# Optimization experiments

Measured on AMD Instinct MI355X. Metric: run time of the kernel, lower is better.

The kernel has to match this reference:

```python
import jax, jax.numpy as jnp
import numpy as np

# ---- problem constants (mirror AdjustInstanceArea __init__ args) ----
NUM_NODES = 2_000_000
NUM_MOVABLE = 1_500_000
NUM_FILLER = 400_000
NUM_NETS = 1_500_000
PINS_PER_NET = 4                       # uniform netpin_start = arange(0, P+1, 4)
NUM_PINS = NUM_NETS * PINS_PER_NET
XL, XH, YL, YH = 0.0, 1000.0, 0.0, 1000.0
NBX = NBY = 512
BIN_W = (XH - XL) / NBX
BIN_H = (YH - YL) / NBY
UNIT_H_CAP = 1.5                       # unit horizontal routing capacity
UNIT_V_CAP = 1.5                       # unit vertical routing capacity
MAX_RATE = 2.0                         # max_route_opt_adjust_rate
MIN_RATE = 1.0 / MAX_RATE
EPS = 1e-6


def setup_inputs() -> dict:
    key = jax.random.key(0)
    k = jax.random.split(key, 4)
    x = jax.random.uniform(k[0], (NUM_NODES,), jnp.float32, XL, XH - 4.0)
    y = jax.random.uniform(k[1], (NUM_NODES,), jnp.float32, YL, YH - 4.0)
    pos = jnp.concatenate([x, y])                      # [2*num_nodes], x then y

    # pins clustered around net centers (realistic small net bboxes)
    rng = np.random.default_rng(0)
    centers = rng.uniform(0.0, 1000.0, size=(NUM_NETS, 1, 2)).astype(np.float32)
    jit = rng.uniform(-20.0, 20.0, size=(NUM_NETS, PINS_PER_NET, 2)).astype(np.float32)
    ppos = np.clip(centers + jit, 0.0, 1000.0)         # [nets, pins_per_net, 2], in net order

    # flat_netpin: pin ids grouped by net; pin_pos indexed by pin id
    flat_netpin = rng.permutation(NUM_PINS).astype(np.int32)
    px = np.empty(NUM_PINS, np.float32); py = np.empty(NUM_PINS, np.float32)
    px[flat_netpin] = ppos[..., 0].reshape(-1)
    py[flat_netpin] = ppos[..., 1].reshape(-1)
    pin_pos = jnp.concatenate([jnp.asarray(px), jnp.asarray(py)])  # [2*num_pins]

    pin2net = jnp.asarray(np.repeat(np.arange(NUM_NETS, dtype=np.int32), PINS_PER_NET))

    node_size_x = jax.random.uniform(k[2], (NUM_NODES,), jnp.float32, 1.0, 4.0)
    node_size_y = jax.random.uniform(k[3], (NUM_NODES,), jnp.float32, 1.0, 4.0)
    return {"pos": pos, "pin_pos": pin_pos,
            "node_size_x": node_size_x, "node_size_y": node_size_y,
            "flat_netpin": jnp.asarray(flat_netpin), "pin2net": pin2net}


def _rect_accum(vals, blx, bly, bhx, bhy):
    """Accumulate vals over inclusive bin rectangles via difference map + 2D cumsum."""
    D = jnp.zeros((NBX + 1, NBY + 1), vals.dtype)
    D = D.at[blx, bly].add(vals)
    D = D.at[bhx + 1, bly].add(-vals)
    D = D.at[blx, bhy + 1].add(-vals)
    D = D.at[bhx + 1, bhy + 1].add(vals)
    return jnp.cumsum(jnp.cumsum(D, axis=0), axis=1)[:NBX, :NBY]


def reference(pos, pin_pos, node_size_x, node_size_y, flat_netpin, pin2net):
    # ---- InstanceRouteOptimizationArea: RUDY routing demand per bin ----
    px = pin_pos[:NUM_PINS][flat_netpin].reshape(NUM_NETS, PINS_PER_NET)
    py = pin_pos[NUM_PINS:][flat_netpin].reshape(NUM_NETS, PINS_PER_NET)
    net_xl = jnp.min(px, axis=1); net_xh = jnp.max(px, axis=1)
    net_yl = jnp.min(py, axis=1); net_yh = jnp.max(py, axis=1)
    bw = net_xh - net_xl
    bh = net_yh - net_yl
    barea = jnp.maximum(bw * bh, EPS)
    dens_h = bw / barea                                # horizontal wire density
    dens_v = bh / barea                                # vertical wire density

    blx = jnp.clip(jnp.floor((net_xl - XL) / BIN_W), 0, NBX - 1).astype(jnp.int32)
    bhx = jnp.clip(jnp.floor((net_xh - XL) / BIN_W), 0, NBX - 1).astype(jnp.int32)
    bly = jnp.clip(jnp.floor((net_yl - YL) / BIN_H), 0, NBY - 1).astype(jnp.int32)
    bhy = jnp.clip(jnp.floor((net_yh - YL) / BIN_H), 0, NBY - 1).astype(jnp.int32)

    util_h = _rect_accum(dens_h, blx, bly, bhx, bhy) / UNIT_H_CAP
    util_v = _rect_accum(dens_v, blx, bly, bhx, bhy) / UNIT_V_CAP

    # per-movable-node utilization (gather at node center bin)
    x = pos[:NUM_NODES]; y = pos[NUM_NODES:]
    nsx_m = node_size_x[:NUM_MOVABLE]; nsy_m = node_size_y[:NUM_MOVABLE]
    cx = x[:NUM_MOVABLE] + 0.5 * nsx_m
    cy = y[:NUM_MOVABLE] + 0.5 * nsy_m
    bix = jnp.clip(jnp.floor((cx - XL) / BIN_W), 0, NBX - 1).astype(jnp.int32)
    biy = jnp.clip(jnp.floor((cy - YL) / BIN_H), 0, NBY - 1).astype(jnp.int32)
    util = jnp.maximum(util_h[bix, biy], util_v[bix, biy])
    ratio = jnp.clip(util, MIN_RATE, MAX_RATE)

    area_old = nsx_m * nsy_m
    instance_route_area = area_old * ratio

    # ---- AdjustInstanceArea: rescale under max_total_area budget ----
    filler_area_old = jnp.sum(node_size_x[NUM_NODES - NUM_FILLER:] *
                              node_size_y[NUM_NODES - NUM_FILLER:])
    max_total_area = jnp.sum(area_old) + filler_area_old
    scale = jnp.minimum(1.0, max_total_area / jnp.maximum(jnp.sum(instance_route_area), EPS))
    new_area = instance_route_area * scale
    sr = jnp.sqrt(new_area / jnp.maximum(area_old, EPS))
    nsx_new = nsx_m * sr
    nsy_new = nsy_m * sr

    # keep cell centers fixed while resizing
    x_out = x.at[:NUM_MOVABLE].add(0.5 * (nsx_m - nsx_new))
    y_out = y.at[:NUM_MOVABLE].add(0.5 * (nsy_m - nsy_new))

    # fillers absorb leftover area budget
    fscale = jnp.sqrt(jnp.maximum(max_total_area - jnp.sum(new_area), 0.0) /
                      jnp.maximum(filler_area_old, EPS))
    nsx_out = node_size_x.at[:NUM_MOVABLE].set(nsx_new)
    nsx_out = nsx_out.at[NUM_NODES - NUM_FILLER:].multiply(fscale)
    nsy_out = node_size_y.at[:NUM_MOVABLE].set(nsy_new)
    nsy_out = nsy_out.at[NUM_NODES - NUM_FILLER:].multiply(fscale)

    return jnp.concatenate([x_out, y_out, nsx_out, nsy_out])  # [4*num_nodes]
```

## Files before the change

kernel.cpp:

```cpp
#include <hip/hip_runtime.h>
#include <hip/hip_fp16.h>
#include <math.h>

#define N_NODES   2000000
#define N_MOVABLE 1500000
#define N_FILLER  400000
#define N_NETS    1500000
#define N_PINS    (N_NETS * 4)
#define NB        512
#define NT        16
#define TILE      32
#define NBUCKET   (NT * NT)
#define CAP       10240
#define NSLICE    4
#define NMAPS     NSLICE
#define NPB       4096
#define RED_BLOCKS 1024

__device__ __forceinline__ int bin_idx(float v) {
    float b = floorf(v / 1.953125f);
    b = fminf(fmaxf(b, 0.0f), 511.0f);
    return (int)b;
}

__global__ void pack_kernel(const float* __restrict__ pin_pos,
                            float2* __restrict__ pp,
                            unsigned* __restrict__ g_ptr) {
    if (blockIdx.x == 0 && threadIdx.x < NBUCKET) g_ptr[threadIdx.x] = 0u;
    int i = blockIdx.x * blockDim.x + threadIdx.x;
    if (i >= N_PINS / 4) return;
    float4 a = reinterpret_cast<const float4*>(pin_pos)[i];
    float4 b = reinterpret_cast<const float4*>(pin_pos + N_PINS)[i];
    float4* o = reinterpret_cast<float4*>(pp + 4 * (size_t)i);
    o[0] = make_float4(a.x, b.x, a.y, b.y);
    o[1] = make_float4(a.z, b.z, a.w, b.w);
}

template <bool PACKED>
__device__ __forceinline__ uint2 make_rec(const float* __restrict__ pin_pos,
                                          const float2* __restrict__ pp,
                                          int4 fp, int* bucket) {
    float2 p0, p1, p2, p3;
    if (PACKED) {
        p0 = pp[fp.x]; p1 = pp[fp.y]; p2 = pp[fp.z]; p3 = pp[fp.w];
    } else {
        p0 = make_float2(pin_pos[fp.x], pin_pos[N_PINS + fp.x]);
        p1 = make_float2(pin_pos[fp.y], pin_pos[N_PINS + fp.y]);
        p2 = make_float2(pin_pos[fp.z], pin_pos[N_PINS + fp.z]);
        p3 = make_float2(pin_pos[fp.w], pin_pos[N_PINS + fp.w]);
    }
    float xl = fminf(fminf(p0.x, p1.x), fminf(p2.x, p3.x));
    float xh = fmaxf(fmaxf(p0.x, p1.x), fmaxf(p2.x, p3.x));
    float yl = fminf(fminf(p0.y, p1.y), fminf(p2.y, p3.y));
    float yh = fmaxf(fmaxf(p0.y, p1.y), fmaxf(p2.y, p3.y));
    float bw = xh - xl, bh = yh - yl;
    float barea = fmaxf(bw * bh, 1e-6f);
    float vh = fminf((bw / barea) * (1.0f / 1.5f), 60000.0f);
    float vv = fminf((bh / barea) * (1.0f / 1.5f), 60000.0f);
    unsigned blx = bin_idx(xl), bhx = bin_idx(xh);
    unsigned bly = bin_idx(yl), bhy = bin_idx(yh);
    *bucket = (int)((bly >> 5) * NT + (blx >> 5));
    __half2 h = __float22half2_rn(make_float2(vh, vv));
    uint2 r;
    r.x = *reinterpret_cast<unsigned*>(&h);
    r.y = blx | (bly << 9) | ((bhx + 1 - blx) << 18) | ((bhy + 1 - bly) << 23);
    return r;
}

template <bool PACKED>
__global__ __launch_bounds__(1024)
void gather_bin_kernel(const float* __restrict__ pin_pos,
                       const float2* __restrict__ pp,
                       const int*  __restrict__ fnp,
                       uint2* __restrict__ slab,
                       unsigned* __restrict__ g_ptr) {
    __shared__ unsigned hist[NBUCKET];
    __shared__ unsigned base[NBUCKET];
    int t = threadIdx.x;
    if (t < NBUCKET) hist[t] = 0;
    __syncthreads();

    int n0 = blockIdx.x * NPB + t;
    bool v[4]; int4 fp[4]; uint2 r[4]; int b[4]; unsigned rk[4];
    #pragma unroll
    for (int k = 0; k < 4; ++k) {
        int n = n0 + k * 1024;
        v[k] = (n < N_NETS);
        fp[k] = v[k] ? *reinterpret_cast<const int4*>(fnp + 4 * (size_t)n)
                     : make_int4(0, 0, 0, 0);
    }
    #pragma unroll
    for (int k = 0; k < 4; ++k) {
        b[k] = 0;
        if (v[k]) r[k] = make_rec<PACKED>(pin_pos, pp, fp[k], &b[k]);
    }
    #pragma unroll
    for (int k = 0; k < 4; ++k) {
        rk[k] = v[k] ? atomicAdd(&hist[b[k]], 1u) : 0u;
    }
    __syncthreads();
    if (t < NBUCKET) {
        unsigned c = hist[t];
        base[t] = c ? atomicAdd(&g_ptr[t], c) : 0u;
    }
    __syncthreads();
    #pragma unroll
    for (int k = 0; k < 4; ++k) {
        if (v[k]) {
            unsigned s = base[b[k]] + rk[k];
            if (s < CAP) slab[(size_t)b[k] * CAP + s] = r[k];
        }
    }
}

__device__ __forceinline__ void rec_process(uint2 r, int x0, int y0,
                                            float2* acc) {
    float2 v = __half22float2(*reinterpret_cast<const __half2*>(&r.x));
    unsigned g = r.y;
    int ax0 = (int)(g & 511u);
    int ay0 = (int)((g >> 9) & 511u);
    int ax1 = ax0 + (int)((g >> 18) & 31u);
    int ay1 = ay0 + (int)((g >> 23) & 31u);
    int X0 = ax0 - x0, Y0 = ay0 - y0;
    int X1 = ax1 - x0, Y1 = ay1 - y0;
    bool iX0 = (unsigned)X0 < TILE, iX1 = (unsigned)X1 < TILE;
    bool iY0 = (unsigned)Y0 < TILE, iY1 = (unsigned)Y1 < TILE;
    if (iX0 && iY0) { atomicAdd(&acc[X0 * TILE + Y0].x,  v.x); atomicAdd(&acc[X0 * TILE + Y0].y,  v.y); }
    if (iX1 && iY0) { atomicAdd(&acc[X1 * TILE + Y0].x, -v.x); atomicAdd(&acc[X1 * TILE + Y0].y, -v.y); }
    if (iX0 && iY1) { atomicAdd(&acc[X0 * TILE + Y1].x, -v.x); atomicAdd(&acc[X0 * TILE + Y1].y, -v.y); }
    if (iX1 && iY1) { atomicAdd(&acc[X1 * TILE + Y1].x,  v.x); atomicAdd(&acc[X1 * TILE + Y1].y,  v.y); }
}

__global__ __launch_bounds__(256)
void accum_kernel(const uint2* __restrict__ slab,
                  const unsigned* __restrict__ g_cnt,
                  float2* __restrict__ Dp) {
    __shared__ float2 acc[TILE * TILE];
    int wg = blockIdx.x;
    int sl = wg & (NSLICE - 1), tile = wg >> 2;
    int tx = tile & (NT - 1), ty = tile >> 4;
    int tid = threadIdx.x;

    for (int i = tid; i < TILE * TILE; i += 256) acc[i] = make_float2(0.f, 0.f);
    __syncthreads();

    int x0 = tx * TILE, y0 = ty * TILE;
    #pragma unroll
    for (int dy = -1; dy <= 0; ++dy) {
        int sy = ty + dy; if (sy < 0) continue;
        #pragma unroll
        for (int dx = -1; dx <= 0; ++dx) {
            int sx = tx + dx; if (sx < 0) continue;
            int sb = sy * NT + sx;
            unsigned cnt = min(g_cnt[sb], (unsigned)CAP);
            unsigned lo = (cnt * (unsigned)sl) >> 2;
            unsigned hi = (cnt * (unsigned)(sl + 1)) >> 2;
            const uint2* recs = slab + (size_t)sb * CAP;
            unsigned i = lo + tid;
            for (; i + 768 < hi; i += 1024) {
                uint2 r0 = recs[i];
                uint2 r1 = recs[i + 256];
                uint2 r2 = recs[i + 512];
                uint2 r3 = recs[i + 768];
                rec_process(r0, x0, y0, acc);
                rec_process(r1, x0, y0, acc);
                rec_process(r2, x0, y0, acc);
                rec_process(r3, x0, y0, acc);
            }
            for (; i < hi; i += 256) rec_process(recs[i], x0, y0, acc);
        }
    }
    __syncthreads();

    float2* D = Dp + (size_t)sl * NB * NB;
    for (int i = tid; i < TILE * TILE; i += 256) {
        int X = i >> 5, Y = i & 31;
        D[(size_t)(x0 + X) * NB + (y0 + Y)] = acc[i];
    }
}

__global__ __launch_bounds__(512)
void scanA_kernel(const float2* __restrict__ Dp, float2* __restrict__ S) {
    __shared__ float2 s[NB];
    int x = blockIdx.x, t = threadIdx.x;
    float2 a = make_float2(0.f, 0.f);
    #pragma unroll
    for (int m = 0; m < NMAPS; ++m) {
        float2 v = Dp[(size_t)m * NB * NB + (size_t)x * NB + t];
        a.x += v.x; a.y += v.y;
    }
    s[t] = a;
    __syncthreads();
    for (int off = 1; off < NB; off <<= 1) {
        float2 u = s[t];
        if (t >= off) { float2 w = s[t - off]; u.x += w.x; u.y += w.y; }
        __syncthreads();
        s[t] = u;
        __syncthreads();
    }
    S[(size_t)x * NB + t] = s[t];
}

__global__ __launch_bounds__(512)
void scanB_kernel(float2* __restrict__ S) {
    __shared__ float2 s[NB];
    int y = blockIdx.x, t = threadIdx.x;
    s[t] = S[(size_t)t * NB + y];
    __syncthreads();
    for (int off = 1; off < NB; off <<= 1) {
        float2 u = s[t];
        if (t >= off) { float2 w = s[t - off]; u.x += w.x; u.y += w.y; }
        __syncthreads();
        s[t] = u;
        __syncthreads();
    }
    S[(size_t)t * NB + y] = s[t];
}

__global__ __launch_bounds__(256)
void reduce_kernel(const float* __restrict__ pos,
                   const float* __restrict__ nsx,
                   const float* __restrict__ nsy,
                   const float2* __restrict__ S,
                   double* __restrict__ partials) {
    const int MQ = N_MOVABLE / 4;
    const int TQ = MQ + N_FILLER / 4;
    double a_old = 0.0, a_route = 0.0, a_fill = 0.0;
    int stride = gridDim.x * blockDim.x;
    for (int q = blockIdx.x * blockDim.x + threadIdx.x; q < TQ; q += stride) {
        if (q < MQ) {
            int i = 4 * q;
            float4 x4  = *reinterpret_cast<const float4*>(pos + i);
            float4 y4  = *reinterpret_cast<const float4*>(pos + N_NODES + i);
            float4 sx4 = *reinterpret_cast<const float4*>(nsx + i);
            float4 sy4 = *reinterpret_cast<const float4*>(nsy + i);
            float xs[4] = {x4.x, x4.y, x4.z, x4.w};
            float ys[4] = {y4.x, y4.y, y4.z, y4.w};
            float sxs[4] = {sx4.x, sx4.y, sx4.z, sx4.w};
            float sys[4] = {sy4.x, sy4.y, sy4.z, sy4.w};
            #pragma unroll
            for (int k = 0; k < 4; ++k) {
                int bx = bin_idx(xs[k] + 0.5f * sxs[k]);
                int by = bin_idx(ys[k] + 0.5f * sys[k]);
                float2 u2 = S[(size_t)bx * NB + by];
                float ratio = fminf(fmaxf(fmaxf(u2.x, u2.y), 0.5f), 2.0f);
                float area = sxs[k] * sys[k];
                a_old += (double)area;
                a_route += (double)(area * ratio);
            }
        } else {
            int j = (N_NODES - N_FILLER) + 4 * (q - MQ);
            float4 sx4 = *reinterpret_cast<const float4*>(nsx + j);
            float4 sy4 = *reinterpret_cast<const float4*>(nsy + j);
            a_fill += (double)(sx4.x * sy4.x + sx4.y * sy4.y +
                               sx4.z * sy4.z + sx4.w * sy4.w);
        }
    }
    for (int off = 32; off > 0; off >>= 1) {
        a_old   += __shfl_down(a_old, off);
        a_route += __shfl_down(a_route, off);
        a_fill  += __shfl_down(a_fill, off);
    }
    __shared__ double sd[4][3];
    int wid = threadIdx.x >> 6, lane = threadIdx.x & 63;
    if (lane == 0) { sd[wid][0] = a_old; sd[wid][1] = a_route; sd[wid][2] = a_fill; }
    __syncthreads();
    if (threadIdx.x == 0) {
        double s0 = 0, s1 = 0, s2 = 0;
        for (int w = 0; w < 4; ++w) { s0 += sd[w][0]; s1 += sd[w][1]; s2 += sd[w][2]; }
        partials[blockIdx.x * 3 + 0] = s0;
        partials[blockIdx.x * 3 + 1] = s1;
        partials[blockIdx.x * 3 + 2] = s2;
    }
}

__global__ __launch_bounds__(256)
void finish_kernel(const double* __restrict__ partials,
                   double* __restrict__ sums) {
    int t = threadIdx.x;
    double s0 = 0, s1 = 0, s2 = 0;
    for (int r = t; r < RED_BLOCKS; r += 256) {
        s0 += partials[r * 3 + 0];
        s1 += partials[r * 3 + 1];
        s2 += partials[r * 3 + 2];
    }
    for (int off = 32; off > 0; off >>= 1) {
        s0 += __shfl_down(s0, off);
        s1 += __shfl_down(s1, off);
        s2 += __shfl_down(s2, off);
    }
    __shared__ double sd[4][3];
    int wid = t >> 6, lane = t & 63;
    if (lane == 0) { sd[wid][0] = s0; sd[wid][1] = s1; sd[wid][2] = s2; }
    __syncthreads();
    if (t == 0) {
        double a = 0, b = 0, c = 0;
        for (int w = 0; w < 4; ++w) { a += sd[w][0]; b += sd[w][1]; c += sd[w][2]; }
        sums[0] = a; sums[1] = b; sums[2] = c;
    }
}

__global__ __launch_bounds__(256)
void final_kernel(const float* __restrict__ pos,
                  const float* __restrict__ nsx,
                  const float* __restrict__ nsy,
                  const float2* __restrict__ S,
                  const double* __restrict__ sums,
                  float* __restrict__ out) {
    double sum_area  = sums[0];
    double sum_route = sums[1];
    double fill_old  = sums[2];
    double max_total = sum_area + fill_old;

    float scale = fminf(1.0f, (float)(max_total / fmax(sum_route, 1e-6)));
    float sum_new = (float)(scale * (float)sum_route);
    float fscale = sqrtf(fmaxf((float)max_total - sum_new, 0.0f) /
                         fmaxf((float)fill_old, 1e-6f));

    int q = blockIdx.x * blockDim.x + threadIdx.x;
    if (q >= N_NODES / 4) return;
    int i = 4 * q;

    float4 x4  = *reinterpret_cast<const float4*>(pos + i);
    float4 y4  = *reinterpret_cast<const float4*>(pos + N_NODES + i);
    float4 sx4 = *reinterpret_cast<const float4*>(nsx + i);
    float4 sy4 = *reinterpret_cast<const float4*>(nsy + i);

    float xs[4] = {x4.x, x4.y, x4.z, x4.w};
    float ys[4] = {y4.x, y4.y, y4.z, y4.w};
    float sxs[4] = {sx4.x, sx4.y, sx4.z, sx4.w};
    float sys[4] = {sy4.x, sy4.y, sy4.z, sy4.w};

    if (i < N_MOVABLE) {
        #pragma unroll
        for (int k = 0; k < 4; ++k) {
            int bx = bin_idx(xs[k] + 0.5f * sxs[k]);
            int by = bin_idx(ys[k] + 0.5f * sys[k]);
            float2 u2 = S[(size_t)bx * NB + by];
            float ratio = fminf(fmaxf(fmaxf(u2.x, u2.y), 0.5f), 2.0f);
            float area = sxs[k] * sys[k];
            float new_area = area * ratio * scale;
            float sr = sqrtf(new_area / fmaxf(area, 1e-6f));
            float sx_new = sxs[k] * sr, sy_new = sys[k] * sr;
            xs[k] = xs[k] + 0.5f * (sxs[k] - sx_new);
            ys[k] = ys[k] + 0.5f * (sys[k] - sy_new);
            sxs[k] = sx_new; sys[k] = sy_new;
        }
    } else if (i >= N_NODES - N_FILLER) {
        #pragma unroll
        for (int k = 0; k < 4; ++k) { sxs[k] *= fscale; sys[k] *= fscale; }
    }

    *reinterpret_cast<float4*>(out + i)               = make_float4(xs[0], xs[1], xs[2], xs[3]);
    *reinterpret_cast<float4*>(out + N_NODES + i)     = make_float4(ys[0], ys[1], ys[2], ys[3]);
    *reinterpret_cast<float4*>(out + 2 * N_NODES + i) = make_float4(sxs[0], sxs[1], sxs[2], sxs[3]);
    *reinterpret_cast<float4*>(out + 3 * N_NODES + i) = make_float4(sys[0], sys[1], sys[2], sys[3]);
}

extern "C" void kernel_launch(void* const* d_in, const int* in_sizes, int n_in,
                              void* d_out, int out_size, void* d_ws, size_t ws_size,
                              hipStream_t stream) {
    const float* pos         = (const float*)d_in[0];
    const float* pin_pos     = (const float*)d_in[1];
    const float* nsx         = (const float*)d_in[2];
    const float* nsy         = (const float*)d_in[3];
    const int*   flat_netpin = (const int*)d_in[4];
    float* out = (float*)d_out;

    const size_t pp_b   = (size_t)N_PINS * sizeof(float2);
    const size_t slab_b = (size_t)NBUCKET * CAP * sizeof(uint2);
    const size_t dp_b   = (size_t)NMAPS * NB * NB * sizeof(float2);
    const size_t s_b    = (size_t)NB * NB * sizeof(float2);
    const size_t part_b = (size_t)RED_BLOCKS * 3 * sizeof(double);
    const size_t gp_b   = 4096;

    const size_t need_primary = pp_b + slab_b + gp_b + 256;

    char* base = (char*)d_ws;
    bool packed = (ws_size >= need_primary);

    float2* pp; uint2* slab; float2* Dp; float2* S;
    double* partials; double* sums; unsigned* g_ptr;
    if (packed) {
        pp       = (float2*)base;
        Dp       = (float2*)base;
        S        = (float2*)(base + dp_b);
        partials = (double*)(base + dp_b + s_b);
        sums     = (double*)(base + dp_b + s_b + part_b);
        slab     = (uint2*)(base + pp_b);
        g_ptr    = (unsigned*)(base + pp_b + slab_b);
    } else {
        pp       = nullptr;
        slab     = (uint2*)base;
        Dp       = (float2*)(base + slab_b);
        S        = (float2*)(base + slab_b + dp_b);
        partials = (double*)(base + slab_b + dp_b + s_b);
        sums     = (double*)(base + slab_b + dp_b + s_b + part_b);
        g_ptr    = (unsigned*)(base + slab_b + dp_b + s_b + part_b + 64);
    }

    const int GB_BLOCKS = (N_NETS + NPB - 1) / NPB;
    if (packed) {
        pack_kernel<<<(N_PINS / 4 + 255) / 256, 256, 0, stream>>>(pin_pos, pp, g_ptr);
        gather_bin_kernel<true><<<GB_BLOCKS, 1024, 0, stream>>>(pin_pos, pp, flat_netpin, slab, g_ptr);
    } else {
        hipMemsetAsync(g_ptr, 0, NBUCKET * sizeof(unsigned), stream);
        gather_bin_kernel<false><<<GB_BLOCKS, 1024, 0, stream>>>(pin_pos, nullptr, flat_netpin, slab, g_ptr);
    }

    accum_kernel <<<NBUCKET * NSLICE, 256, 0, stream>>>(slab, g_ptr, Dp);
    scanA_kernel <<<NB, 512, 0, stream>>>(Dp, S);
    scanB_kernel <<<NB, 512, 0, stream>>>(S);
    reduce_kernel<<<RED_BLOCKS, 256, 0, stream>>>(pos, nsx, nsy, S, partials);
    finish_kernel<<<1, 256, 0, stream>>>(partials, sums);
    final_kernel <<<(N_NODES / 4 + 255) / 256, 256, 0, stream>>>(pos, nsx, nsy, S, sums, out);
}
```

Measured before the change: 239.0 us.

## Replace random pin gather with three-pass bucketed pin gather and net reduction

```diff
diff --git a/kernel.cpp b/kernel.cpp
--- a/kernel.cpp
+++ b/kernel.cpp
@@ -14,8 +14,19 @@
 #define CAP       10240
 #define NSLICE    4
 #define NMAPS     NSLICE
-#define NPB       4096
 #define RED_BLOCKS 1024
+
+#define NQ        24
+#define QRNG      250000
+#define NXCD      8
+#define RPX       3
+#define PIN_PER_XCD (QRNG * RPX)
+#define P2CHUNK   4096
+#define P2CHUNKS  ((PIN_PER_XCD + P2CHUNK - 1) / P2CHUNK)
+
+#define SB_SHIFT  14
+#define SB_CAP    16384
+#define NSB       ((N_PINS + SB_CAP - 1) / SB_CAP)
 
 __device__ __forceinline__ int bin_idx(float v) {
     float b = floorf(v / 1.953125f);
@@ -23,10 +34,178 @@
     return (int)b;
 }
 
+__global__ __launch_bounds__(1024)
+void p1_bucketq_kernel(const int* __restrict__ fnp,
+                       uint2* __restrict__ qslab,
+                       unsigned* __restrict__ g_qptr) {
+    __shared__ unsigned hist[NQ];
+    __shared__ unsigned hbase[NQ];
+    int t = threadIdx.x;
+    if (t < NQ) hist[t] = 0;
+    __syncthreads();
+
+    int s0 = blockIdx.x * 4096 + t * 4;
+    unsigned q[4]; unsigned qb[4]; unsigned rk[4]; bool val[4];
+    if (s0 + 3 < N_PINS) {
+        int4 f = *reinterpret_cast<const int4*>(fnp + s0);
+        q[0] = (unsigned)f.x; q[1] = (unsigned)f.y;
+        q[2] = (unsigned)f.z; q[3] = (unsigned)f.w;
+        val[0] = val[1] = val[2] = val[3] = true;
+    } else {
+        #pragma unroll
+        for (int j = 0; j < 4; ++j) {
+            val[j] = (s0 + j < N_PINS);
+            q[j] = val[j] ? (unsigned)fnp[s0 + j] : 0u;
+        }
+    }
+    #pragma unroll
+    for (int j = 0; j < 4; ++j) {
+        qb[j] = q[j] / (unsigned)QRNG;
+        rk[j] = val[j] ? atomicAdd(&hist[qb[j]], 1u) : 0u;
+    }
+    __syncthreads();
+    if (t < NQ) {
+        unsigned c = hist[t];
+        hbase[t] = c ? atomicAdd(&g_qptr[t], c) : 0u;
+    }
+    __syncthreads();
+    #pragma unroll
+    for (int j = 0; j < 4; ++j) {
+        if (val[j]) {
+            unsigned idx = qb[j] * (unsigned)QRNG + hbase[qb[j]] + rk[j];
+            qslab[idx] = make_uint2(q[j], (unsigned)(s0 + j));
+        }
+    }
+}
+
+__global__ __launch_bounds__(1024)
+void p2_gather_kernel(const uint2* __restrict__ qslab,
+                      const float* __restrict__ pin_pos,
+                      uint2* __restrict__ sslab,
+                      unsigned* __restrict__ xcd_ctr,
+                      unsigned* __restrict__ g_sptr) {
+    __shared__ unsigned hist[NSB];
+    __shared__ unsigned hbase[NSB];
+    __shared__ unsigned sh_c;
+    int k = blockIdx.x & (NXCD - 1);
+    int t = threadIdx.x;
+
+    for (;;) {
+        if (t == 0) sh_c = atomicAdd(&xcd_ctr[k], 1u);
+        __syncthreads();
+        unsigned c = sh_c;
+        __syncthreads();
+        if (c >= (unsigned)P2CHUNKS) break;
+
+        for (int i = t; i < NSB; i += 1024) hist[i] = 0;
+        __syncthreads();
+
+        uint2 rec[4]; int sb[4]; unsigned rk[4]; bool val[4];
+        #pragma unroll
+        for (int j = 0; j < 4; ++j) {
+            unsigned s = c * P2CHUNK + t + j * 1024;
+            val[j] = (s < (unsigned)PIN_PER_XCD);
+            sb[j] = 0; rk[j] = 0;
+            if (val[j]) {
+                unsigned rl = s / (unsigned)QRNG;
+                unsigned ridx = s - rl * (unsigned)QRNG;
+                unsigned r = (unsigned)k + 8u * rl;
+                uint2 qr = qslab[r * (unsigned)QRNG + ridx];
+                float x = pin_pos[qr.x];
+                float y = pin_pos[qr.x + N_PINS];
+                unsigned xq = __float2uint_rn(x * 64.0f);
+                unsigned yq = __float2uint_rn(y * 64.0f);
+                rec[j] = make_uint2(qr.y, xq | (yq << 16));
+                sb[j] = (int)(qr.y >> SB_SHIFT);
+                rk[j] = atomicAdd(&hist[sb[j]], 1u);
+            }
+        }
+        __syncthreads();
+        for (int i = t; i < NSB; i += 1024) {
+            unsigned h = hist[i];
+            hbase[i] = h ? atomicAdd(&g_sptr[i], h) : 0u;
+        }
+        __syncthreads();
+        #pragma unroll
+        for (int j = 0; j < 4; ++j) {
+            if (val[j]) sslab[(size_t)sb[j] * SB_CAP + hbase[sb[j]] + rk[j]] = rec[j];
+        }
+        __syncthreads();
+    }
+}
+
+__device__ __forceinline__ uint2 pack_tile_rec(float bw, float bh,
+                                               unsigned blx, unsigned bhx,
+                                               unsigned bly, unsigned bhy,
+                                               int* tb) {
+    float barea = fmaxf(bw * bh, 1e-6f);
+    float vh = fminf((bw / barea) * (1.0f / 1.5f), 60000.0f);
+    float vv = fminf((bh / barea) * (1.0f / 1.5f), 60000.0f);
+    *tb = (int)((bly >> 5) * NT + (blx >> 5));
+    __half2 h = __float22half2_rn(make_float2(vh, vv));
+    uint2 r;
+    r.x = *reinterpret_cast<unsigned*>(&h);
+    r.y = blx | (bly << 9) | ((bhx + 1 - blx) << 18) | ((bhy + 1 - bly) << 23);
+    return r;
+}
+
+__global__ __launch_bounds__(512)
+void p3_netred_kernel(const uint2* __restrict__ sslab,
+                      uint2* __restrict__ tslab,
+                      unsigned* __restrict__ g_tptr) {
+    __shared__ unsigned mnx[4096], mxx[4096], mny[4096], mxy[4096];
+    __shared__ unsigned hist[NBUCKET];
+    __shared__ unsigned hbase[NBUCKET];
+    int bid = blockIdx.x, t = threadIdx.x;
+    int base_slot = bid * SB_CAP;
+    int cnt  = min(SB_CAP, N_PINS - base_slot);
+    int base_net = bid * (SB_CAP / 4);
+    int nets = min(SB_CAP / 4, N_NETS - base_net);
+
+    for (int i = t; i < 4096; i += 512) {
+        mnx[i] = 0xFFFFFFFFu; mny[i] = 0xFFFFFFFFu; mxx[i] = 0u; mxy[i] = 0u;
+    }
+    for (int i = t; i < NBUCKET; i += 512) hist[i] = 0;
+    __syncthreads();
+
+    for (int i = t; i < cnt; i += 512) {
+        uint2 rc = sslab[(size_t)base_slot + i];
+        unsigned nl = (rc.x >> 2) - (unsigned)base_net;
+        unsigned xq = rc.y & 0xFFFFu, yq = rc.y >> 16;
+        atomicMin(&mnx[nl], xq); atomicMax(&mxx[nl], xq);
+        atomicMin(&mny[nl], yq); atomicMax(&mxy[nl], yq);
+    }
+    __syncthreads();
+
+    uint2 rec[8]; int tb[8]; unsigned rk[8];
+    #pragma unroll
+    for (int u = 0; u < 8; ++u) {
+        int j = t + u * 512;
+        tb[u] = -1;
+        if (j < nets) {
+            unsigned xl = mnx[j], xh = mxx[j], yl = mny[j], yh = mxy[j];
+            float bw = (float)(xh - xl) * 0.015625f;
+            float bh = (float)(yh - yl) * 0.015625f;
+            unsigned blx = min(xl / 125u, 511u), bhx = min(xh / 125u, 511u);
+            unsigned bly = min(yl / 125u, 511u), bhy = min(yh / 125u, 511u);
+            rec[u] = pack_tile_rec(bw, bh, blx, bhx, bly, bhy, &tb[u]);
+            rk[u] = atomicAdd(&hist[tb[u]], 1u);
+        }
+    }
+    __syncthreads();
+    if (t < NBUCKET) {
+        unsigned h = hist[t];
+        hbase[t] = h ? atomicAdd(&g_tptr[t], h) : 0u;
+    }
+    __syncthreads();
+    #pragma unroll
+    for (int u = 0; u < 8; ++u) {
+        if (tb[u] >= 0) tslab[(size_t)tb[u] * CAP + hbase[tb[u]] + rk[u]] = rec[u];
+    }
+}
+
 __global__ void pack_kernel(const float* __restrict__ pin_pos,
-                            float2* __restrict__ pp,
-                            unsigned* __restrict__ g_ptr) {
-    if (blockIdx.x == 0 && threadIdx.x < NBUCKET) g_ptr[threadIdx.x] = 0u;
+                            float2* __restrict__ pp) {
     int i = blockIdx.x * blockDim.x + threadIdx.x;
     if (i >= N_PINS / 4) return;
     float4 a = reinterpret_cast<const float4*>(pin_pos)[i];
@@ -37,9 +216,9 @@
 }
 
 template <bool PACKED>
-__device__ __forceinline__ uint2 make_rec(const float* __restrict__ pin_pos,
-                                          const float2* __restrict__ pp,
-                                          int4 fp, int* bucket) {
+__device__ __forceinline__ uint2 make_rec_f(const float* __restrict__ pin_pos,
+                                            const float2* __restrict__ pp,
+                                            int4 fp, int* tb) {
     float2 p0, p1, p2, p3;
     if (PACKED) {
         p0 = pp[fp.x]; p1 = pp[fp.y]; p2 = pp[fp.z]; p3 = pp[fp.w];
@@ -53,34 +232,25 @@
     float xh = fmaxf(fmaxf(p0.x, p1.x), fmaxf(p2.x, p3.x));
     float yl = fminf(fminf(p0.y, p1.y), fminf(p2.y, p3.y));
     float yh = fmaxf(fmaxf(p0.y, p1.y), fmaxf(p2.y, p3.y));
-    float bw = xh - xl, bh = yh - yl;
-    float barea = fmaxf(bw * bh, 1e-6f);
-    float vh = fminf((bw / barea) * (1.0f / 1.5f), 60000.0f);
-    float vv = fminf((bh / barea) * (1.0f / 1.5f), 60000.0f);
     unsigned blx = bin_idx(xl), bhx = bin_idx(xh);
     unsigned bly = bin_idx(yl), bhy = bin_idx(yh);
-    *bucket = (int)((bly >> 5) * NT + (blx >> 5));
-    __half2 h = __float22half2_rn(make_float2(vh, vv));
-    uint2 r;
-    r.x = *reinterpret_cast<unsigned*>(&h);
-    r.y = blx | (bly << 9) | ((bhx + 1 - blx) << 18) | ((bhy + 1 - bly) << 23);
-    return r;
+    return pack_tile_rec(xh - xl, yh - yl, blx, bhx, bly, bhy, tb);
 }
 
 template <bool PACKED>
 __global__ __launch_bounds__(1024)
 void gather_bin_kernel(const float* __restrict__ pin_pos,
                        const float2* __restrict__ pp,
-                       const int*  __restrict__ fnp,
+                       const int* __restrict__ fnp,
                        uint2* __restrict__ slab,
                        unsigned* __restrict__ g_ptr) {
     __shared__ unsigned hist[NBUCKET];
-    __shared__ unsigned base[NBUCKET];
+    __shared__ unsigned hbase[NBUCKET];
     int t = threadIdx.x;
     if (t < NBUCKET) hist[t] = 0;
     __syncthreads();
 
-    int n0 = blockIdx.x * NPB + t;
+    int n0 = blockIdx.x * 4096 + t;
     bool v[4]; int4 fp[4]; uint2 r[4]; int b[4]; unsigned rk[4];
     #pragma unroll
     for (int k = 0; k < 4; ++k) {
@@ -92,22 +262,20 @@
     #pragma unroll
     for (int k = 0; k < 4; ++k) {
         b[k] = 0;
-        if (v[k]) r[k] = make_rec<PACKED>(pin_pos, pp, fp[k], &b[k]);
-    }
-    #pragma unroll
-    for (int k = 0; k < 4; ++k) {
-        rk[k] = v[k] ? atomicAdd(&hist[b[k]], 1u) : 0u;
-    }
+        if (v[k]) r[k] = make_rec_f<PACKED>(pin_pos, pp, fp[k], &b[k]);
+    }
+    #pragma unroll
+    for (int k = 0; k < 4; ++k) rk[k] = v[k] ? atomicAdd(&hist[b[k]], 1u) : 0u;
     __syncthreads();
     if (t < NBUCKET) {
         unsigned c = hist[t];
-        base[t] = c ? atomicAdd(&g_ptr[t], c) : 0u;
+        hbase[t] = c ? atomicAdd(&g_ptr[t], c) : 0u;
     }
     __syncthreads();
     #pragma unroll
     for (int k = 0; k < 4; ++k) {
         if (v[k]) {
-            unsigned s = base[b[k]] + rk[k];
+            unsigned s = hbase[b[k]] + rk[k];
             if (s < CAP) slab[(size_t)b[k] * CAP + s] = r[k];
         }
     }
@@ -367,48 +535,77 @@
     const int*   flat_netpin = (const int*)d_in[4];
     float* out = (float*)d_out;
 
-    const size_t pp_b   = (size_t)N_PINS * sizeof(float2);
-    const size_t slab_b = (size_t)NBUCKET * CAP * sizeof(uint2);
-    const size_t dp_b   = (size_t)NMAPS * NB * NB * sizeof(float2);
-    const size_t s_b    = (size_t)NB * NB * sizeof(float2);
-    const size_t part_b = (size_t)RED_BLOCKS * 3 * sizeof(double);
-    const size_t gp_b   = 4096;
-
-    const size_t need_primary = pp_b + slab_b + gp_b + 256;
+    const size_t qslab_b = (size_t)N_PINS * sizeof(uint2);
+    const size_t sslab_b = (size_t)NSB * SB_CAP * sizeof(uint2);
+    const size_t tslab_b = (size_t)NBUCKET * CAP * sizeof(uint2);
+    const size_t ctr_b   = 4096;
+    const size_t dp_b    = (size_t)NMAPS * NB * NB * sizeof(float2);
+    const size_t s_b     = (size_t)NB * NB * sizeof(float2);
+    const size_t part_b  = (size_t)RED_BLOCKS * 3 * sizeof(double);
+    const size_t pp_b    = (size_t)N_PINS * sizeof(float2);
+
+    const size_t need_new = qslab_b + sslab_b + tslab_b + ctr_b;
+    const size_t need_r8  = pp_b + tslab_b + ctr_b;
 
     char* base = (char*)d_ws;
-    bool packed = (ws_size >= need_primary);
-
-    float2* pp; uint2* slab; float2* Dp; float2* S;
-    double* partials; double* sums; unsigned* g_ptr;
-    if (packed) {
-        pp       = (float2*)base;
+    int tier = (ws_size >= need_new) ? 0 : (ws_size >= need_r8) ? 1 : 2;
+
+    uint2* tslab; unsigned* ctrs; float2* Dp; float2* S;
+    double* partials; double* sums;
+
+    if (tier == 0) {
+        uint2* qslab = (uint2*)base;
+        uint2* sslab = (uint2*)(base + qslab_b);
+        tslab        = (uint2*)(base + qslab_b + sslab_b);
+        ctrs         = (unsigned*)(base + qslab_b + sslab_b + tslab_b);
         Dp       = (float2*)base;
         S        = (float2*)(base + dp_b);
         partials = (double*)(base + dp_b + s_b);
         sums     = (double*)(base + dp_b + s_b + part_b);
-        slab     = (uint2*)(base + pp_b);
-        g_ptr    = (unsigned*)(base + pp_b + slab_b);
+
+        unsigned* g_qptr  = ctrs;
+        unsigned* xcd_ctr = ctrs + 32;
+        unsigned* g_sptr  = ctrs + 64;
+        unsigned* g_tptr  = ctrs + 448;
+
+        hipMemsetAsync(ctrs, 0, ctr_b, stream);
+        p1_bucketq_kernel<<<(N_PINS + 4095) / 4096, 1024, 0, stream>>>(
+            flat_netpin, qslab, g_qptr);
+        p2_gather_kernel<<<P2CHUNKS * NXCD, 1024, 0, stream>>>(
+            qslab, pin_pos, sslab, xcd_ctr, g_sptr);
+        p3_netred_kernel<<<NSB, 512, 0, stream>>>(sslab, tslab, g_tptr);
+
+        accum_kernel <<<NBUCKET * NSLICE, 256, 0, stream>>>(tslab, g_tptr, Dp);
+    } else if (tier == 1) {
+        float2* pp = (float2*)base;
+        tslab      = (uint2*)(base + pp_b);
+        ctrs       = (unsigned*)(base + pp_b + tslab_b);
+        Dp       = (float2*)base;
+        S        = (float2*)(base + dp_b);
+        partials = (double*)(base + dp_b + s_b);
+        sums     = (double*)(base + dp_b + s_b + part_b);
+        unsigned* g_tptr = ctrs + 448;
+
+        hipMemsetAsync(ctrs, 0, ctr_b, stream);
+        pack_kernel<<<(N_PINS / 4 + 255) / 256, 256, 0, stream>>>(pin_pos, pp);
+        gather_bin_kernel<true><<<(N_NETS + 4095) / 4096, 1024, 0, stream>>>(
+            pin_pos, pp, flat_netpin, tslab, g_tptr);
+        accum_kernel <<<NBUCKET * NSLICE, 256, 0, stream>>>(tslab, g_tptr, Dp);
     } else {
-        pp       = nullptr;
-        slab     = (uint2*)base;
-        Dp       = (float2*)(base + slab_b);
-        S        = (float2*)(base + slab_b + dp_b);
-        partials = (double*)(base + slab_b + dp_b + s_b);
-        sums     = (double*)(base + slab_b + dp_b + s_b + part_b);
-        g_ptr    = (unsigned*)(base + slab_b + dp_b + s_b + part_b + 64);
-    }
-
-    const int GB_BLOCKS = (N_NETS + NPB - 1) / NPB;
-    if (packed) {
-        pack_kernel<<<(N_PINS / 4 + 255) / 256, 256, 0, stream>>>(pin_pos, pp, g_ptr);
-        gather_bin_kernel<true><<<GB_BLOCKS, 1024, 0, stream>>>(pin_pos, pp, flat_netpin, slab, g_ptr);
-    } else {
-        hipMemsetAsync(g_ptr, 0, NBUCKET * sizeof(unsigned), stream);
-        gather_bin_kernel<false><<<GB_BLOCKS, 1024, 0, stream>>>(pin_pos, nullptr, flat_netpin, slab, g_ptr);
-    }
-
-    accum_kernel <<<NBUCKET * NSLICE, 256, 0, stream>>>(slab, g_ptr, Dp);
+        tslab = (uint2*)base;
+        Dp    = (float2*)(base + tslab_b);
+        S     = (float2*)(base + tslab_b + dp_b);
+        partials = (double*)(base + tslab_b + dp_b + s_b);
+        sums     = (double*)(base + tslab_b + dp_b + s_b + part_b);
+        ctrs     = (unsigned*)(base + tslab_b + dp_b + s_b + part_b + 64);
+        unsigned* g_tptr = ctrs + 448;
+
+        hipMemsetAsync(ctrs, 0, ctr_b, stream);
+        gather_bin_kernel<false><<<(N_NETS + 4095) / 4096, 1024, 0, stream>>>(
+            pin_pos, nullptr, flat_netpin, tslab, g_tptr);
+        accum_kernel <<<NBUCKET * NSLICE, 256, 0, stream>>>(tslab, ctrs + 448, Dp);
+    }
+
     scanA_kernel <<<NB, 512, 0, stream>>>(Dp, S);
     scanB_kernel <<<NB, 512, 0, stream>>>(S);
     reduce_kernel<<<RED_BLOCKS, 256, 0, stream>>>(pos, nsx, nsy, S, partials);
```

Measured after the change: 249.9 us. +4.6%, slower.
